# Optimization experiments

Measured on AMD Instinct MI355X. Metric: run time of the kernel, lower is better.

## Reference

```python
import jax, jax.numpy as jnp
import numpy as np

N_NODES = 100000
N_EDGES = 1600000
IN_FEAT = 256
HIDDEN = 64
N_CLASSES = 16


def gcn_conv(x, edge_index, W, b):
    """PyG GCNConv: add self-loops, symmetric normalization, linear+aggregate."""
    n = x.shape[0]
    src, dst = edge_index[0], edge_index[1]
    loops = jnp.arange(n, dtype=src.dtype)
    src = jnp.concatenate([src, loops])
    dst = jnp.concatenate([dst, loops])
    # in-degree on graph with self-loops
    deg = jax.ops.segment_sum(jnp.ones(src.shape[0], dtype=x.dtype), dst, num_segments=n)
    dinv = jnp.where(deg > 0, jax.lax.rsqrt(deg), 0.0)
    h = x @ W                                  # [N, out]
    norm = dinv[src] * dinv[dst]               # [E+N]
    msg = h[src] * norm[:, None]                # gather + scale (memory-bound)
    out = jax.ops.segment_sum(msg, dst, num_segments=n)  # scatter-add
    return out + b


def setup_inputs() -> dict:
    key = jax.random.key(0)
    ks = jax.random.split(key, 5)
    x = jax.random.normal(ks[0], (N_NODES, IN_FEAT), dtype=jnp.float32)
    edge_index = jax.random.randint(ks[1], (2, N_EDGES), 0, N_NODES, dtype=jnp.int64)
    W1 = jax.random.normal(ks[2], (IN_FEAT, HIDDEN), dtype=jnp.float32) * (1.0 / np.sqrt(IN_FEAT))
    b1 = jnp.zeros((HIDDEN,), dtype=jnp.float32)
    W2 = jax.random.normal(ks[3], (HIDDEN, N_CLASSES), dtype=jnp.float32) * (1.0 / np.sqrt(HIDDEN))
    b2 = jnp.zeros((N_CLASSES,), dtype=jnp.float32)
    return {"x": x, "edge_index": edge_index, "W1": W1, "b1": b1, "W2": W2, "b2": b2}


def reference(x, edge_index, W1, b1, W2, b2):
    h = gcn_conv(x, edge_index, W1, b1)
    h = jax.nn.relu(h)
    # dropout p=0.5 is identity in eval mode (training=False)
    out = gcn_conv(h, edge_index, W2, b2)
    return out
```

## Files before the change

kernel.cpp:

```cpp
#include <hip/hip_runtime.h>

#define NN 100000
#define NE 1600000
#define FIN 256
#define FH 64
#define FC 16

#define SCAN_CHUNK 1024
#define NB_SCAN ((NN + SCAN_CHUNK - 1) / SCAN_CHUNK)
#define NB_COUNT ((NE + 255) / 256)
#define NB_GEMM1 ((NN + 127) / 128)
#define NB_FUSED (9 * NB_GEMM1)

typedef int v2i __attribute__((ext_vector_type(2)));
typedef short s16x8 __attribute__((ext_vector_type(8)));
typedef float f32x4 __attribute__((ext_vector_type(4)));

__device__ __forceinline__ float4 fma4(float4 v, float w, float4 a) {
    a.x = fmaf(v.x, w, a.x); a.y = fmaf(v.y, w, a.y);
    a.z = fmaf(v.z, w, a.z); a.w = fmaf(v.w, w, a.w);
    return a;
}
__device__ __forceinline__ float4 add4(float4 a, float4 v) {
    a.x += v.x; a.y += v.y; a.z += v.z; a.w += v.w;
    return a;
}
__device__ __forceinline__ float4 xor_add4(float4 r, int m) {
    r.x += __shfl_xor(r.x, m, 64); r.y += __shfl_xor(r.y, m, 64);
    r.z += __shfl_xor(r.z, m, 64); r.w += __shfl_xor(r.w, m, 64);
    return r;
}

__device__ __forceinline__ unsigned short bf16rne(float f) {
    unsigned u = __float_as_uint(f);
    u += 0x7FFFu + ((u >> 16) & 1u);
    return (unsigned short)(u >> 16);
}

__device__ __forceinline__ void split8(const float* f, s16x8& hi, s16x8& lo) {
    #pragma unroll
    for (int i = 0; i < 8; i++) {
        unsigned u = __float_as_uint(f[i]);
        unsigned short h = (unsigned short)((u + 0x7FFFu + ((u >> 16) & 1u)) >> 16);
        float l = f[i] - __uint_as_float((unsigned)h << 16);
        unsigned ul = __float_as_uint(l);
        hi[i] = (short)h;
        lo[i] = (short)((ul + 0x7FFFu + ((ul >> 16) & 1u)) >> 16);
    }
}

__device__ __forceinline__ int eidx(const int* __restrict__ ei, int f, int pos) {
    return f ? ei[2 * pos] : ei[pos];
}

__global__ __launch_bounds__(256) void prep_k(const int* __restrict__ ei,
                                              int* __restrict__ flag,
                                              const float* __restrict__ W,
                                              unsigned short* __restrict__ Whi,
                                              unsigned short* __restrict__ Wlo) {
    int b = blockIdx.x;
    if (b == 8) {
        if (threadIdx.x == 0) {
            int z = (ei[1] == 0) & (ei[3] == 0) & (ei[5] == 0) & (ei[7] == 0);
            *flag = z;
        }
        return;
    }
    int slot = b * 256 + threadIdx.x;
    int l = slot & 63;
    int c = (slot >> 6) & 3;
    int s = slot >> 8;
    int k0 = s * 32 + (l >> 4) * 8;
    int col = c * 16 + (l & 15);
    #pragma unroll
    for (int i = 0; i < 8; i++) {
        float f = W[(k0 + i) * FH + col];
        unsigned short h = bf16rne(f);
        float lres = f - __uint_as_float((unsigned)h << 16);
        Whi[slot * 8 + i] = h;
        Wlo[slot * 8 + i] = bf16rne(lres);
    }
}

__global__ __launch_bounds__(256, 4) void fused_k(const int* __restrict__ ei,
                                                  const int* __restrict__ flag,
                                                  int* __restrict__ deg,
                                                  v2i* __restrict__ packed,
                                                  const float* __restrict__ x,
                                                  const unsigned short* __restrict__ Whi,
                                                  const unsigned short* __restrict__ Wlo,
                                                  float* __restrict__ h1) {
    const int b = blockIdx.x;
    if ((b % 9) != 8) {
        int cb = (b / 9) * 8 + (b % 9);
        if (cb >= NB_COUNT) return;
        int e = cb * 256 + threadIdx.x;
        if (e >= NE) return;
        int f = *flag;
        int s = eidx(ei, f, e);
        int d = eidx(ei, f, NE + e);
        int r = atomicAdd(&deg[d], 1);
        v2i p; p.x = s; p.y = d | (r << 17);
        packed[e] = p;
        return;
    }
    const int t = threadIdx.x;
    const int lane = t & 63;
    const int wid = t >> 6;
    const int mb = (b / 9) * 128 + wid * 32;
    const int lr = lane & 15;
    const int lk = (lane >> 4) * 8;

    int ra0 = mb + lr;
    int ra1 = mb + 16 + lr;
    const float* pa0 = x + (size_t)(ra0 < NN ? ra0 : NN - 1) * FIN + lk;
    const float* pa1 = x + (size_t)(ra1 < NN ? ra1 : NN - 1) * FIN + lk;

    f32x4 acc[2][4] = {};

    for (int s = 0; s < 8; s++) {
        float fa0[8], fa1[8];
        float4 q;
        q = *(const float4*)(pa0 + s * 32);
        fa0[0] = q.x; fa0[1] = q.y; fa0[2] = q.z; fa0[3] = q.w;
        q = *(const float4*)(pa0 + s * 32 + 4);
        fa0[4] = q.x; fa0[5] = q.y; fa0[6] = q.z; fa0[7] = q.w;
        q = *(const float4*)(pa1 + s * 32);
        fa1[0] = q.x; fa1[1] = q.y; fa1[2] = q.z; fa1[3] = q.w;
        q = *(const float4*)(pa1 + s * 32 + 4);
        fa1[4] = q.x; fa1[5] = q.y; fa1[6] = q.z; fa1[7] = q.w;

        s16x8 a0h, a0l, a1h, a1l;
        split8(fa0, a0h, a0l);
        split8(fa1, a1h, a1l);

        #pragma unroll
        for (int c = 0; c < 4; c++) {
            s16x8 wh = *(const s16x8*)&Whi[((s * 4 + c) * 64 + lane) * 8];
            s16x8 wl = *(const s16x8*)&Wlo[((s * 4 + c) * 64 + lane) * 8];
            acc[0][c] = __builtin_amdgcn_mfma_f32_16x16x32_bf16(a0h, wh, acc[0][c], 0, 0, 0);
            acc[0][c] = __builtin_amdgcn_mfma_f32_16x16x32_bf16(a0l, wh, acc[0][c], 0, 0, 0);
            acc[0][c] = __builtin_amdgcn_mfma_f32_16x16x32_bf16(a0h, wl, acc[0][c], 0, 0, 0);
            acc[1][c] = __builtin_amdgcn_mfma_f32_16x16x32_bf16(a1h, wh, acc[1][c], 0, 0, 0);
            acc[1][c] = __builtin_amdgcn_mfma_f32_16x16x32_bf16(a1l, wh, acc[1][c], 0, 0, 0);
            acc[1][c] = __builtin_amdgcn_mfma_f32_16x16x32_bf16(a1h, wl, acc[1][c], 0, 0, 0);
        }
    }
    #pragma unroll
    for (int r = 0; r < 2; r++) {
        int rowb = mb + 16 * r + (lane >> 4) * 4;
        #pragma unroll
        for (int c = 0; c < 4; c++) {
            #pragma unroll
            for (int v = 0; v < 4; v++) {
                int row = rowb + v;
                if (row < NN)
                    h1[(size_t)row * FH + 16 * c + lr] = acc[r][c][v];
            }
        }
    }
}

__global__ __launch_bounds__(256) void scan_sum_k(const int* __restrict__ deg,
                                                  int* __restrict__ partial,
                                                  float* __restrict__ dinv) {
    __shared__ int red[256];
    int b = blockIdx.x, t = threadIdx.x;
    int base = b * SCAN_CHUNK + t * 4;
    int s = 0;
    #pragma unroll
    for (int i = 0; i < 4; i++) {
        int idx = base + i;
        if (idx < NN) {
            int dv = deg[idx];
            s += dv;
            dinv[idx] = rsqrtf((float)(dv + 1));
        }
    }
    red[t] = s;
    __syncthreads();
    for (int off = 128; off > 0; off >>= 1) {
        if (t < off) red[t] += red[t + off];
        __syncthreads();
    }
    if (t == 0) partial[b] = red[0];
}

__global__ __launch_bounds__(256) void scale1_k(float* __restrict__ h1,
                                                const float* __restrict__ dinv) {
    int i = blockIdx.x * 256 + threadIdx.x;
    if (i >= NN * 16) return;
    int row = i >> 4;
    float d = dinv[row];
    float4 v = *(const float4*)&h1[i * 4];
    v.x *= d; v.y *= d; v.z *= d; v.w *= d;
    *(float4*)&h1[i * 4] = v;
}

__global__ __launch_bounds__(128) void scan_part_k(int* __restrict__ partial) {
    __shared__ int s[128];
    int t = threadIdx.x;
    int v = (t < NB_SCAN) ? partial[t] : 0;
    s[t] = v; __syncthreads();
    for (int off = 1; off < 128; off <<= 1) {
        int u = (t >= off) ? s[t - off] : 0;
        __syncthreads();
        s[t] += u;
        __syncthreads();
    }
    if (t < NB_SCAN) partial[t] = s[t] - v;
}

__global__ __launch_bounds__(256) void scan_out_k(const int* __restrict__ deg,
                                                  const int* __restrict__ partial,
                                                  int* __restrict__ row_start) {
    __shared__ int s[256];
    int b = blockIdx.x, t = threadIdx.x;
    int base = b * SCAN_CHUNK + t * 4;
    int v[4]; int sum = 0;
    #pragma unroll
    for (int i = 0; i < 4; i++) {
        int idx = base + i;
        v[i] = (idx < NN) ? deg[idx] : 0;
        sum += v[i];
    }
    s[t] = sum; __syncthreads();
    for (int off = 1; off < 256; off <<= 1) {
        int u = (t >= off) ? s[t - off] : 0;
        __syncthreads();
        s[t] += u;
        __syncthreads();
    }
    int run = partial[b] + s[t] - sum;
    #pragma unroll
    for (int i = 0; i < 4; i++) {
        int idx = base + i;
        if (idx < NN) {
            row_start[idx] = run;
            run += v[i];
            if (idx == NN - 1) row_start[NN] = run;
        }
    }
}

__global__ __launch_bounds__(256) void fill_k(const v2i* __restrict__ packed,
                                              const int* __restrict__ row_start,
                                              int* __restrict__ csr) {
    int e = blockIdx.x * 256 + threadIdx.x;
    if (e >= NE) return;
    v2i p = __builtin_nontemporal_load(&packed[e]);
    int d = p.y & 0x1FFFF;
    int r = ((unsigned)p.y) >> 17;
    csr[row_start[d] + r] = p.x;
}

__global__ __launch_bounds__(256) void agg1g_k(const int* __restrict__ csr,
                                               const int* __restrict__ row_start,
                                               const float* __restrict__ h1,
                                               const float* __restrict__ dinv,
                                               const float* __restrict__ b1,
                                               const float* __restrict__ W2,
                                               float* __restrict__ h2) {
    __shared__ float sW2[FH * FC];
    __shared__ float sp[4][FH];
    const int t = threadIdx.x;
    #pragma unroll
    for (int i = 0; i < 4; i++) sW2[t + 256 * i] = W2[t + 256 * i];
    __syncthreads();

    int wid = t >> 6;
    int n = blockIdx.x * 4 + wid;
    int lane = t & 63;
    if (n >= NN) return;
    int sg = lane >> 4;
    int fl = lane & 15;
    int s0 = row_start[n], s1 = row_start[n + 1];
    float4 A = make_float4(0.f, 0.f, 0.f, 0.f);
    float4 B = make_float4(0.f, 0.f, 0.f, 0.f);
    float4 C = make_float4(0.f, 0.f, 0.f, 0.f);
    float4 D = make_float4(0.f, 0.f, 0.f, 0.f);
    for (int j0 = s0; j0 < s1; j0 += 64) {
        int idx = j0 + lane;
        int sl = (idx < s1) ? csr[idx] : 0;
        int cnt = s1 - j0; if (cnt > 64) cnt = 64;
        int j = 0;
        for (; j + 16 <= cnt; j += 16) {
            int eA = __shfl(sl, j + sg, 64);
            int eB = __shfl(sl, j + 4 + sg, 64);
            int eC = __shfl(sl, j + 8 + sg, 64);
            int eD = __shfl(sl, j + 12 + sg, 64);
            float4 vA = *(const float4*)&h1[eA * FH + fl * 4];
            float4 vB = *(const float4*)&h1[eB * FH + fl * 4];
            float4 vC = *(const float4*)&h1[eC * FH + fl * 4];
            float4 vD = *(const float4*)&h1[eD * FH + fl * 4];
            A = add4(A, vA); B = add4(B, vB);
            C = add4(C, vC); D = add4(D, vD);
        }
        if (j + 8 <= cnt) {
            int eA = __shfl(sl, j + sg, 64);
            int eB = __shfl(sl, j + 4 + sg, 64);
            float4 vA = *(const float4*)&h1[eA * FH + fl * 4];
            float4 vB = *(const float4*)&h1[eB * FH + fl * 4];
            A = add4(A, vA); B = add4(B, vB);
            j += 8;
        }
        if (j + 4 <= cnt) {
            int eA = __shfl(sl, j + sg, 64);
            float4 vA = *(const float4*)&h1[eA * FH + fl * 4];
            A = add4(A, vA);
            j += 4;
        }
        int rem = cnt - j;
        if (rem > 0) {
            int jj = j + (sg < rem ? sg : 0);
            int eA = __shfl(sl, jj, 64);
            float wA = (sg < rem) ? 1.f : 0.f;
            float4 vA = *(const float4*)&h1[eA * FH + fl * 4];
            A = fma4(vA, wA, A);
        }
    }
    float4 r = add4(add4(A, B), add4(C, D));
    r = xor_add4(r, 16);
    r = xor_add4(r, 32);
    float dn = dinv[n];
    if (sg == 0) {
        float4 self = *(const float4*)&h1[n * FH + fl * 4];
        float4 bq = *(const float4*)&b1[fl * 4];
        float4 p;
        p.x = fmaxf(fmaf(r.x + self.x, dn, bq.x), 0.f);
        p.y = fmaxf(fmaf(r.y + self.y, dn, bq.y), 0.f);
        p.z = fmaxf(fmaf(r.z + self.z, dn, bq.z), 0.f);
        p.w = fmaxf(fmaf(r.w + self.w, dn, bq.w), 0.f);
        *(float4*)&sp[wid][fl * 4] = p;
    }
    __builtin_amdgcn_s_waitcnt(0);
    if (lane < FC) {
        float o = 0.f;
        #pragma unroll 8
        for (int k = 0; k < FH; k++)
            o = fmaf(sp[wid][k], sW2[k * FC + lane], o);
        h2[n * FC + lane] = o * dn;
    }
}

__global__ __launch_bounds__(256) void agg2_k(const int* __restrict__ csr,
                                              const int* __restrict__ row_start,
                                              const float* __restrict__ h2,
                                              const float* __restrict__ dinv,
                                              const float* __restrict__ b2,
                                              float* __restrict__ out) {
    const int t = threadIdx.x;
    int n = blockIdx.x * 16 + (t >> 4);
    int l16 = t & 15;
    int base = t & 48;
    int q = (t >> 2) & 3;
    int c = t & 3;
    if (n >= NN) return;
    int s0 = row_start[n], s1 = row_start[n + 1];
    float4 A = make_float4(0.f, 0.f, 0.f, 0.f);
    float4 B = make_float4(0.f, 0.f, 0.f, 0.f);
    float4 C = make_float4(0.f, 0.f, 0.f, 0.f);
    float4 D = make_float4(0.f, 0.f, 0.f, 0.f);
    for (int j0 = s0; j0 < s1; j0 += 16) {
        int idx = j0 + l16;
        int sl = (idx < s1) ? csr[idx] : 0;
        int cnt = s1 - j0; if (cnt > 16) cnt = 16;
        int j = 0;
        if (j + 16 <= cnt) {
            int eA = __shfl(sl, base + j + q, 64);
            int eB = __shfl(sl, base + j + 4 + q, 64);
            int eC = __shfl(sl, base + j + 8 + q, 64);
            int eD = __shfl(sl, base + j + 12 + q, 64);
            float4 vA = *(const float4*)&h2[eA * FC + c * 4];
            float4 vB = *(const float4*)&h2[eB * FC + c * 4];
            float4 vC = *(const float4*)&h2[eC * FC + c * 4];
            float4 vD = *(const float4*)&h2[eD * FC + c * 4];
            A = add4(A, vA); B = add4(B, vB);
            C = add4(C, vC); D = add4(D, vD);
            j += 16;
        }
        if (j + 8 <= cnt) {
            int eA = __shfl(sl, base + j + q, 64);
            int eB = __shfl(sl, base + j + 4 + q, 64);
            float4 vA = *(const float4*)&h2[eA * FC + c * 4];
            float4 vB = *(const float4*)&h2[eB * FC + c * 4];
            A = add4(A, vA); B = add4(B, vB);
            j += 8;
        }
        if (j + 4 <= cnt) {
            int eA = __shfl(sl, base + j + q, 64);
            float4 vA = *(const float4*)&h2[eA * FC + c * 4];
            A = add4(A, vA);
            j += 4;
        }
        int rem = cnt - j;
        if (rem > 0) {
            int jj = base + j + (q < rem ? q : 0);
            int eA = __shfl(sl, jj, 64);
            float wA = (q < rem) ? 1.f : 0.f;
            float4 vA = *(const float4*)&h2[eA * FC + c * 4];
            A = fma4(vA, wA, A);
        }
    }
    float4 r = add4(add4(A, B), add4(C, D));
    r = xor_add4(r, 4);
    r = xor_add4(r, 8);
    if (q == 0) {
        float dn = dinv[n];
        float4 self = *(const float4*)&h2[n * FC + c * 4];
        float4 bq = *(const float4*)&b2[c * 4];
        float4 p;
        p.x = fmaf(r.x + self.x, dn, bq.x);
        p.y = fmaf(r.y + self.y, dn, bq.y);
        p.z = fmaf(r.z + self.z, dn, bq.z);
        p.w = fmaf(r.w + self.w, dn, bq.w);
        *(float4*)&out[n * FC + c * 4] = p;
    }
}

extern "C" void kernel_launch(void* const* d_in, const int* in_sizes, int n_in,
                              void* d_out, int out_size, void* d_ws, size_t ws_size,
                              hipStream_t stream) {
    const float* x  = (const float*)d_in[0];
    const int*   ei = (const int*)d_in[1];
    const float* W1 = (const float*)d_in[2];
    const float* b1 = (const float*)d_in[3];
    const float* W2 = (const float*)d_in[4];
    const float* b2 = (const float*)d_in[5];
    float* out = (float*)d_out;

    char* ws = (char*)d_ws;
    int*   deg       = (int*)(ws + 0);
    int*   row_start = (int*)(ws + 512 * 1024);
    float* dinv      = (float*)(ws + 1024 * 1024);
    int*   flag      = (int*)(ws + 1536 * 1024);
    int*   partial   = (int*)(ws + 1540 * 1024);
    unsigned short* Whi = (unsigned short*)(ws + 1544 * 1024);
    unsigned short* Wlo = (unsigned short*)(ws + 1584 * 1024);
    int*   csr       = (int*)(ws + 2ull * 1024 * 1024);
    float* h1        = (float*)(ws + 9ull * 1024 * 1024);
    v2i*   packed    = (v2i*)(ws + 35ull * 1024 * 1024);
    float* h2        = (float*)(ws + 35ull * 1024 * 1024);

    prep_k<<<9, 256, 0, stream>>>(ei, flag, W1, Whi, Wlo);
    (void)hipMemsetAsync(deg, 0, NN * sizeof(int), stream);
    fused_k<<<NB_FUSED, 256, 0, stream>>>(ei, flag, deg, packed, x, Whi, Wlo, h1);
    scan_sum_k<<<NB_SCAN, 256, 0, stream>>>(deg, partial, dinv);
    scale1_k<<<(NN * 16 + 255) / 256, 256, 0, stream>>>(h1, dinv);
    scan_part_k<<<1, 128, 0, stream>>>(partial);
    scan_out_k<<<NB_SCAN, 256, 0, stream>>>(deg, partial, row_start);
    fill_k<<<(NE + 255) / 256, 256, 0, stream>>>(packed, row_start, csr);

    agg1g_k<<<(NN + 3) / 4, 256, 0, stream>>>(csr, row_start, h1, dinv, b1, W2, h2);
    agg2_k<<<(NN + 15) / 16, 256, 0, stream>>>(csr, row_start, h2, dinv, b2, out);
}
```

Baseline: 353.9 us.

## Vectorize edge counting and CSR fill, fuse h1 scaling into scan-sum kernel

The degree-counting blocks now have each thread handle four edges with vector loads of the edge indices and packed stores, so the fused kernel's block interleave ratio drops from 8:1 to 2:1. The fill kernel handles two edges per thread with a 16-byte nontemporal load. The separate scale1 kernel is removed, and h1 rows are scaled by dinv inside scan_sum_k using a shared-memory copy of dinv. This saves one launch and one pass over h1. The cost is fewer, heavier blocks and a scan kernel that now streams about 25 MB of h1 with only 98 blocks, which may underuse the GPU.

```diff
diff --git a/kernel.cpp b/kernel.cpp
--- a/kernel.cpp
+++ b/kernel.cpp
@@ -8,11 +8,12 @@
 
 #define SCAN_CHUNK 1024
 #define NB_SCAN ((NN + SCAN_CHUNK - 1) / SCAN_CHUNK)
-#define NB_COUNT ((NE + 255) / 256)
+#define NB_COUNT ((NE / 4 + 255) / 256)
 #define NB_GEMM1 ((NN + 127) / 128)
-#define NB_FUSED (9 * NB_GEMM1)
+#define NB_FUSED (3 * NB_GEMM1)
 
 typedef int v2i __attribute__((ext_vector_type(2)));
+typedef int v4i __attribute__((ext_vector_type(4)));
 typedef short s16x8 __attribute__((ext_vector_type(8)));
 typedef float f32x4 __attribute__((ext_vector_type(4)));
 
@@ -47,10 +48,6 @@
         hi[i] = (short)h;
         lo[i] = (short)((ul + 0x7FFFu + ((ul >> 16) & 1u)) >> 16);
     }
-}
-
-__device__ __forceinline__ int eidx(const int* __restrict__ ei, int f, int pos) {
-    return f ? ei[2 * pos] : ei[pos];
 }
 
 __global__ __launch_bounds__(256) void prep_k(const int* __restrict__ ei,
@@ -91,23 +88,43 @@
                                                   const unsigned short* __restrict__ Wlo,
                                                   float* __restrict__ h1) {
     const int b = blockIdx.x;
-    if ((b % 9) != 8) {
-        int cb = (b / 9) * 8 + (b % 9);
+    if ((b % 3) != 2) {
+        int cb = (b / 3) * 2 + (b % 3);
         if (cb >= NB_COUNT) return;
-        int e = cb * 256 + threadIdx.x;
+        int e = (cb * 256 + threadIdx.x) * 4;
         if (e >= NE) return;
         int f = *flag;
-        int s = eidx(ei, f, e);
-        int d = eidx(ei, f, NE + e);
-        int r = atomicAdd(&deg[d], 1);
-        v2i p; p.x = s; p.y = d | (r << 17);
-        packed[e] = p;
+        int s0, s1, s2, s3, d0, d1, d2, d3;
+        if (f) {
+            v4i a = *(const v4i*)&ei[2 * e];
+            v4i b2 = *(const v4i*)&ei[2 * e + 4];
+            s0 = a.x; s1 = a.z; s2 = b2.x; s3 = b2.z;
+            v4i c = *(const v4i*)&ei[2 * (NE + e)];
+            v4i d = *(const v4i*)&ei[2 * (NE + e) + 4];
+            d0 = c.x; d1 = c.z; d2 = d.x; d3 = d.z;
+        } else {
+            v4i a = *(const v4i*)&ei[e];
+            s0 = a.x; s1 = a.y; s2 = a.z; s3 = a.w;
+            v4i c = *(const v4i*)&ei[NE + e];
+            d0 = c.x; d1 = c.y; d2 = c.z; d3 = c.w;
+        }
+        int r0 = atomicAdd(&deg[d0], 1);
+        int r1 = atomicAdd(&deg[d1], 1);
+        int r2 = atomicAdd(&deg[d2], 1);
+        int r3 = atomicAdd(&deg[d3], 1);
+        v4i pa, pb;
+        pa.x = s0; pa.y = d0 | (r0 << 17);
+        pa.z = s1; pa.w = d1 | (r1 << 17);
+        pb.x = s2; pb.y = d2 | (r2 << 17);
+        pb.z = s3; pb.w = d3 | (r3 << 17);
+        *(v4i*)&packed[e] = pa;
+        *(v4i*)&packed[e + 2] = pb;
         return;
     }
     const int t = threadIdx.x;
     const int lane = t & 63;
     const int wid = t >> 6;
-    const int mb = (b / 9) * 128 + wid * 32;
+    const int mb = (b / 3) * 128 + wid * 32;
     const int lr = lane & 15;
     const int lk = (lane >> 4) * 8;
 
@@ -163,38 +180,44 @@
 
 __global__ __launch_bounds__(256) void scan_sum_k(const int* __restrict__ deg,
                                                   int* __restrict__ partial,
-                                                  float* __restrict__ dinv) {
+                                                  float* __restrict__ dinv,
+                                                  float* __restrict__ h1) {
     __shared__ int red[256];
+    __shared__ float sdv[SCAN_CHUNK];
     int b = blockIdx.x, t = threadIdx.x;
     int base = b * SCAN_CHUNK + t * 4;
     int s = 0;
     #pragma unroll
     for (int i = 0; i < 4; i++) {
         int idx = base + i;
+        float dv = 0.f;
         if (idx < NN) {
-            int dv = deg[idx];
-            s += dv;
-            dinv[idx] = rsqrtf((float)(dv + 1));
-        }
+            int d = deg[idx];
+            s += d;
+            dv = rsqrtf((float)(d + 1));
+            dinv[idx] = dv;
+        }
+        sdv[t * 4 + i] = dv;
     }
     red[t] = s;
     __syncthreads();
+    #pragma unroll 4
+    for (int it = 0; it < 64; it++) {
+        int q = it * 256 + t;
+        int rl = q >> 4;
+        int row = b * SCAN_CHUNK + rl;
+        if (row < NN) {
+            float d = sdv[rl];
+            float4 v = *(const float4*)&h1[(size_t)row * FH + (q & 15) * 4];
+            v.x *= d; v.y *= d; v.z *= d; v.w *= d;
+            *(float4*)&h1[(size_t)row * FH + (q & 15) * 4] = v;
+        }
+    }
     for (int off = 128; off > 0; off >>= 1) {
         if (t < off) red[t] += red[t + off];
         __syncthreads();
     }
     if (t == 0) partial[b] = red[0];
-}
-
-__global__ __launch_bounds__(256) void scale1_k(float* __restrict__ h1,
-                                                const float* __restrict__ dinv) {
-    int i = blockIdx.x * 256 + threadIdx.x;
-    if (i >= NN * 16) return;
-    int row = i >> 4;
-    float d = dinv[row];
-    float4 v = *(const float4*)&h1[i * 4];
-    v.x *= d; v.y *= d; v.z *= d; v.w *= d;
-    *(float4*)&h1[i * 4] = v;
 }
 
 __global__ __launch_bounds__(128) void scan_part_k(int* __restrict__ partial) {
@@ -243,15 +266,18 @@
     }
 }
 
-__global__ __launch_bounds__(256) void fill_k(const v2i* __restrict__ packed,
+__global__ __launch_bounds__(256) void fill_k(const int* __restrict__ packed,
                                               const int* __restrict__ row_start,
                                               int* __restrict__ csr) {
-    int e = blockIdx.x * 256 + threadIdx.x;
+    int e = (blockIdx.x * 256 + threadIdx.x) * 2;
     if (e >= NE) return;
-    v2i p = __builtin_nontemporal_load(&packed[e]);
-    int d = p.y & 0x1FFFF;
-    int r = ((unsigned)p.y) >> 17;
-    csr[row_start[d] + r] = p.x;
+    v4i p = __builtin_nontemporal_load((const v4i*)&packed[2 * e]);
+    int d0 = p.y & 0x1FFFF;
+    int r0 = ((unsigned)p.y) >> 17;
+    int d1 = p.w & 0x1FFFF;
+    int r1 = ((unsigned)p.w) >> 17;
+    csr[row_start[d0] + r0] = p.x;
+    csr[row_start[d1] + r1] = p.z;
 }
 
 __global__ __launch_bounds__(256) void agg1g_k(const int* __restrict__ csr,
@@ -445,11 +471,10 @@
     prep_k<<<9, 256, 0, stream>>>(ei, flag, W1, Whi, Wlo);
     (void)hipMemsetAsync(deg, 0, NN * sizeof(int), stream);
     fused_k<<<NB_FUSED, 256, 0, stream>>>(ei, flag, deg, packed, x, Whi, Wlo, h1);
-    scan_sum_k<<<NB_SCAN, 256, 0, stream>>>(deg, partial, dinv);
-    scale1_k<<<(NN * 16 + 255) / 256, 256, 0, stream>>>(h1, dinv);
+    scan_sum_k<<<NB_SCAN, 256, 0, stream>>>(deg, partial, dinv, h1);
     scan_part_k<<<1, 128, 0, stream>>>(partial);
     scan_out_k<<<NB_SCAN, 256, 0, stream>>>(deg, partial, row_start);
-    fill_k<<<(NE + 255) / 256, 256, 0, stream>>>(packed, row_start, csr);
+    fill_k<<<(NE / 2 + 255) / 256, 256, 0, stream>>>((const int*)packed, row_start, csr);
 
     agg1g_k<<<(NN + 3) / 4, 256, 0, stream>>>(csr, row_start, h1, dinv, b1, W2, h2);
     agg2_k<<<(NN + 15) / 16, 256, 0, stream>>>(csr, row_start, h2, dinv, b2, out);
```

Result: slower. 368.9 us (+4.2%).

## Replace atomic-degree CSR build with two-level bucket sort by destination

Applied to the files above, without the earlier changes.

Builds the CSR with a two-level counting sort instead of global per-node atomics plus a packed fill pass. Edges are first histogrammed and scattered into 512-node buckets using shared-memory atomics. A per-bucket kernel then builds local histograms, row starts, dinv and the CSR in LDS, and also applies the dinv scaling to h1. This removes the global atomic contention, the memset, several scan kernels and the separate scale pass, but unfuses the GEMM from edge counting and reads edge_index twice. CSR order within a row is no longer deterministic.

```diff
diff --git a/kernel.cpp b/kernel.cpp
--- a/kernel.cpp
+++ b/kernel.cpp
@@ -6,13 +6,15 @@
 #define FH 64
 #define FC 16
 
-#define SCAN_CHUNK 1024
-#define NB_SCAN ((NN + SCAN_CHUNK - 1) / SCAN_CHUNK)
-#define NB_COUNT ((NE + 255) / 256)
+#define NPB 512
+#define NBKT ((NN + NPB - 1) / NPB)
+#define NBLK 256
+#define CHUNK (NE / NBLK)
+#define CAP 12288
 #define NB_GEMM1 ((NN + 127) / 128)
-#define NB_FUSED (9 * NB_GEMM1)
 
 typedef int v2i __attribute__((ext_vector_type(2)));
+typedef int v4i __attribute__((ext_vector_type(4)));
 typedef short s16x8 __attribute__((ext_vector_type(8)));
 typedef float f32x4 __attribute__((ext_vector_type(4)));
 
@@ -36,7 +38,6 @@
     u += 0x7FFFu + ((u >> 16) & 1u);
     return (unsigned short)(u >> 16);
 }
-
 __device__ __forceinline__ void split8(const float* f, s16x8& hi, s16x8& lo) {
     #pragma unroll
     for (int i = 0; i < 8; i++) {
@@ -47,10 +48,6 @@
         hi[i] = (short)h;
         lo[i] = (short)((ul + 0x7FFFu + ((ul >> 16) & 1u)) >> 16);
     }
-}
-
-__device__ __forceinline__ int eidx(const int* __restrict__ ei, int f, int pos) {
-    return f ? ei[2 * pos] : ei[pos];
 }
 
 __global__ __launch_bounds__(256) void prep_k(const int* __restrict__ ei,
@@ -82,32 +79,14 @@
     }
 }
 
-__global__ __launch_bounds__(256, 4) void fused_k(const int* __restrict__ ei,
-                                                  const int* __restrict__ flag,
-                                                  int* __restrict__ deg,
-                                                  v2i* __restrict__ packed,
-                                                  const float* __restrict__ x,
+__global__ __launch_bounds__(256, 4) void gemm1_k(const float* __restrict__ x,
                                                   const unsigned short* __restrict__ Whi,
                                                   const unsigned short* __restrict__ Wlo,
                                                   float* __restrict__ h1) {
-    const int b = blockIdx.x;
-    if ((b % 9) != 8) {
-        int cb = (b / 9) * 8 + (b % 9);
-        if (cb >= NB_COUNT) return;
-        int e = cb * 256 + threadIdx.x;
-        if (e >= NE) return;
-        int f = *flag;
-        int s = eidx(ei, f, e);
-        int d = eidx(ei, f, NE + e);
-        int r = atomicAdd(&deg[d], 1);
-        v2i p; p.x = s; p.y = d | (r << 17);
-        packed[e] = p;
-        return;
-    }
     const int t = threadIdx.x;
     const int lane = t & 63;
     const int wid = t >> 6;
-    const int mb = (b / 9) * 128 + wid * 32;
+    const int mb = blockIdx.x * 128 + wid * 32;
     const int lr = lane & 15;
     const int lk = (lane >> 4) * 8;
 
@@ -161,97 +140,142 @@
     }
 }
 
-__global__ __launch_bounds__(256) void scan_sum_k(const int* __restrict__ deg,
-                                                  int* __restrict__ partial,
-                                                  float* __restrict__ dinv) {
-    __shared__ int red[256];
-    int b = blockIdx.x, t = threadIdx.x;
-    int base = b * SCAN_CHUNK + t * 4;
-    int s = 0;
-    #pragma unroll
-    for (int i = 0; i < 4; i++) {
-        int idx = base + i;
-        if (idx < NN) {
-            int dv = deg[idx];
-            s += dv;
-            dinv[idx] = rsqrtf((float)(dv + 1));
-        }
-    }
-    red[t] = s;
-    __syncthreads();
-    for (int off = 128; off > 0; off >>= 1) {
-        if (t < off) red[t] += red[t + off];
-        __syncthreads();
-    }
-    if (t == 0) partial[b] = red[0];
-}
-
-__global__ __launch_bounds__(256) void scale1_k(float* __restrict__ h1,
-                                                const float* __restrict__ dinv) {
-    int i = blockIdx.x * 256 + threadIdx.x;
-    if (i >= NN * 16) return;
-    int row = i >> 4;
-    float d = dinv[row];
-    float4 v = *(const float4*)&h1[i * 4];
-    v.x *= d; v.y *= d; v.z *= d; v.w *= d;
-    *(float4*)&h1[i * 4] = v;
-}
-
-__global__ __launch_bounds__(128) void scan_part_k(int* __restrict__ partial) {
-    __shared__ int s[128];
-    int t = threadIdx.x;
-    int v = (t < NB_SCAN) ? partial[t] : 0;
-    s[t] = v; __syncthreads();
-    for (int off = 1; off < 128; off <<= 1) {
+__global__ __launch_bounds__(256) void hist_k(const int* __restrict__ ei,
+                                              const int* __restrict__ flag,
+                                              int* __restrict__ cnt) {
+    __shared__ int hist[NBKT];
+    const int t = threadIdx.x, blk = blockIdx.x;
+    for (int j = t; j < NBKT; j += 256) hist[j] = 0;
+    __syncthreads();
+    int f = *flag;
+    int base = blk * CHUNK;
+    if (f) {
+        for (int i = t; i < CHUNK; i += 256) {
+            v2i p = *(const v2i*)&ei[2 * (NE + base + i)];
+            atomicAdd(&hist[p.x >> 9], 1);
+        }
+    } else {
+        for (int i = t; i < CHUNK; i += 256) {
+            int d = ei[NE + base + i];
+            atomicAdd(&hist[d >> 9], 1);
+        }
+    }
+    __syncthreads();
+    for (int j = t; j < NBKT; j += 256) cnt[j * NBLK + blk] = hist[j];
+}
+
+__global__ __launch_bounds__(1024) void scanoff_k(int* __restrict__ cnt,
+                                                  int* __restrict__ bucketBase) {
+    __shared__ int s[1024];
+    const int t = threadIdx.x;
+    const int SEG = (NBKT * NBLK) / 1024;
+    int base = t * SEG;
+    int sum = 0;
+    for (int i = 0; i < SEG; i++) sum += cnt[base + i];
+    s[t] = sum; __syncthreads();
+    for (int off = 1; off < 1024; off <<= 1) {
         int u = (t >= off) ? s[t - off] : 0;
         __syncthreads();
         s[t] += u;
         __syncthreads();
     }
-    if (t < NB_SCAN) partial[t] = s[t] - v;
-}
-
-__global__ __launch_bounds__(256) void scan_out_k(const int* __restrict__ deg,
-                                                  const int* __restrict__ partial,
-                                                  int* __restrict__ row_start) {
-    __shared__ int s[256];
-    int b = blockIdx.x, t = threadIdx.x;
-    int base = b * SCAN_CHUNK + t * 4;
-    int v[4]; int sum = 0;
-    #pragma unroll
-    for (int i = 0; i < 4; i++) {
-        int idx = base + i;
-        v[i] = (idx < NN) ? deg[idx] : 0;
-        sum += v[i];
-    }
-    s[t] = sum; __syncthreads();
+    int run = s[t] - sum;
+    for (int i = 0; i < SEG; i++) {
+        int g = base + i;
+        int v = cnt[g];
+        cnt[g] = run;
+        if ((g & (NBLK - 1)) == 0) bucketBase[g / NBLK] = run;
+        run += v;
+    }
+    if (t == 0) bucketBase[NBKT] = NE;
+}
+
+__global__ __launch_bounds__(256) void scat_k(const int* __restrict__ ei,
+                                              const int* __restrict__ flag,
+                                              const int* __restrict__ cnt,
+                                              int* __restrict__ sorted) {
+    __shared__ int offl[NBKT];
+    const int t = threadIdx.x, blk = blockIdx.x;
+    for (int j = t; j < NBKT; j += 256) offl[j] = cnt[j * NBLK + blk];
+    __syncthreads();
+    int f = *flag;
+    int base = blk * CHUNK;
+    if (f) {
+        for (int i = t; i < CHUNK; i += 256) {
+            int e = base + i;
+            v2i ps = *(const v2i*)&ei[2 * e];
+            v2i pd = *(const v2i*)&ei[2 * (NE + e)];
+            int s = ps.x, d = pd.x;
+            int pos = atomicAdd(&offl[d >> 9], 1);
+            sorted[pos] = s | ((d & (NPB - 1)) << 17);
+        }
+    } else {
+        for (int i = t; i < CHUNK; i += 256) {
+            int e = base + i;
+            int s = ei[e], d = ei[NE + e];
+            int pos = atomicAdd(&offl[d >> 9], 1);
+            sorted[pos] = s | ((d & (NPB - 1)) << 17);
+        }
+    }
+}
+
+__global__ __launch_bounds__(256) void bucket_k(const int* __restrict__ sorted,
+                                                const int* __restrict__ bucketBase,
+                                                int* __restrict__ csr,
+                                                int* __restrict__ row_start,
+                                                float* __restrict__ dinv,
+                                                float* __restrict__ h1) {
+    __shared__ int stash[CAP];
+    __shared__ int hist[NPB];
+    __shared__ int startl[NPB];
+    __shared__ int cursor[NPB];
+    __shared__ int ss[256];
+    const int t = threadIdx.x, b = blockIdx.x;
+    const int nb0 = b * NPB;
+    const int ncnt = (NN - nb0 < NPB) ? (NN - nb0) : NPB;
+    const int ebase = bucketBase[b];
+    const int ecnt = bucketBase[b + 1] - ebase;
+
+    hist[t] = 0; hist[t + 256] = 0;
+    __syncthreads();
+    for (int i = t; i < ecnt; i += 256) {
+        int v = sorted[ebase + i];
+        if (i < CAP) stash[i] = v;
+        atomicAdd(&hist[v >> 17], 1);
+    }
+    __syncthreads();
+    int a = hist[2 * t], c = hist[2 * t + 1];
+    int p = a + c;
+    ss[t] = p; __syncthreads();
     for (int off = 1; off < 256; off <<= 1) {
-        int u = (t >= off) ? s[t - off] : 0;
+        int u = (t >= off) ? ss[t - off] : 0;
         __syncthreads();
-        s[t] += u;
+        ss[t] += u;
         __syncthreads();
     }
-    int run = partial[b] + s[t] - sum;
-    #pragma unroll
-    for (int i = 0; i < 4; i++) {
-        int idx = base + i;
-        if (idx < NN) {
-            row_start[idx] = run;
-            run += v[i];
-            if (idx == NN - 1) row_start[NN] = run;
-        }
-    }
-}
-
-__global__ __launch_bounds__(256) void fill_k(const v2i* __restrict__ packed,
-                                              const int* __restrict__ row_start,
-                                              int* __restrict__ csr) {
-    int e = blockIdx.x * 256 + threadIdx.x;
-    if (e >= NE) return;
-    v2i p = __builtin_nontemporal_load(&packed[e]);
-    int d = p.y & 0x1FFFF;
-    int r = ((unsigned)p.y) >> 17;
-    csr[row_start[d] + r] = p.x;
+    int ex = ss[t] - p;
+    startl[2 * t] = ex;       startl[2 * t + 1] = ex + a;
+    cursor[2 * t] = ex;       cursor[2 * t + 1] = ex + a;
+    __syncthreads();
+    for (int j = t; j < ncnt; j += 256) {
+        row_start[nb0 + j] = ebase + startl[j];
+        dinv[nb0 + j] = rsqrtf((float)(hist[j] + 1));
+    }
+    if (b == 0 && t == 0) row_start[NN] = NE;
+    for (int i = t; i < ecnt; i += 256) {
+        int v = (i < CAP) ? stash[i] : sorted[ebase + i];
+        int dl = v >> 17;
+        int r = atomicAdd(&cursor[dl], 1);
+        csr[ebase + r] = v & 0x1FFFF;
+    }
+    for (int q = t; q < ncnt * 16; q += 256) {
+        int rl = q >> 4;
+        float dv = rsqrtf((float)(hist[rl] + 1));
+        size_t off = (size_t)(nb0 + rl) * FH + (q & 15) * 4;
+        float4 v = *(const float4*)&h1[off];
+        v.x *= dv; v.y *= dv; v.z *= dv; v.w *= dv;
+        *(float4*)&h1[off] = v;
+    }
 }
 
 __global__ __launch_bounds__(256) void agg1g_k(const int* __restrict__ csr,
@@ -430,26 +454,24 @@
     float* out = (float*)d_out;
 
     char* ws = (char*)d_ws;
-    int*   deg       = (int*)(ws + 0);
-    int*   row_start = (int*)(ws + 512 * 1024);
-    float* dinv      = (float*)(ws + 1024 * 1024);
-    int*   flag      = (int*)(ws + 1536 * 1024);
-    int*   partial   = (int*)(ws + 1540 * 1024);
-    unsigned short* Whi = (unsigned short*)(ws + 1544 * 1024);
-    unsigned short* Wlo = (unsigned short*)(ws + 1584 * 1024);
-    int*   csr       = (int*)(ws + 2ull * 1024 * 1024);
-    float* h1        = (float*)(ws + 9ull * 1024 * 1024);
-    v2i*   packed    = (v2i*)(ws + 35ull * 1024 * 1024);
-    float* h2        = (float*)(ws + 35ull * 1024 * 1024);
+    int*   row_start  = (int*)(ws + 0);
+    float* dinv       = (float*)(ws + 512ull * 1024);
+    int*   flag       = (int*)(ws + 1024ull * 1024);
+    int*   bucketBase = (int*)(ws + 1028ull * 1024);
+    unsigned short* Whi = (unsigned short*)(ws + 1040ull * 1024);
+    unsigned short* Wlo = (unsigned short*)(ws + 1072ull * 1024);
+    int*   cnt        = (int*)(ws + 1104ull * 1024);
+    int*   csr        = (int*)(ws + 2048ull * 1024);
+    int*   sorted     = (int*)(ws + 9216ull * 1024);
+    float* h2         = (float*)(ws + 9216ull * 1024);
+    float* h1         = (float*)(ws + 16384ull * 1024);
 
     prep_k<<<9, 256, 0, stream>>>(ei, flag, W1, Whi, Wlo);
-    (void)hipMemsetAsync(deg, 0, NN * sizeof(int), stream);
-    fused_k<<<NB_FUSED, 256, 0, stream>>>(ei, flag, deg, packed, x, Whi, Wlo, h1);
-    scan_sum_k<<<NB_SCAN, 256, 0, stream>>>(deg, partial, dinv);
-    scale1_k<<<(NN * 16 + 255) / 256, 256, 0, stream>>>(h1, dinv);
-    scan_part_k<<<1, 128, 0, stream>>>(partial);
-    scan_out_k<<<NB_SCAN, 256, 0, stream>>>(deg, partial, row_start);
-    fill_k<<<(NE + 255) / 256, 256, 0, stream>>>(packed, row_start, csr);
+    gemm1_k<<<NB_GEMM1, 256, 0, stream>>>(x, Whi, Wlo, h1);
+    hist_k<<<NBLK, 256, 0, stream>>>(ei, flag, cnt);
+    scanoff_k<<<1, 1024, 0, stream>>>(cnt, bucketBase);
+    scat_k<<<NBLK, 256, 0, stream>>>(ei, flag, cnt, sorted);
+    bucket_k<<<NBKT, 256, 0, stream>>>(sorted, bucketBase, csr, row_start, dinv, h1);
 
     agg1g_k<<<(NN + 3) / 4, 256, 0, stream>>>(csr, row_start, h1, dinv, b1, W2, h2);
     agg2_k<<<(NN + 15) / 16, 256, 0, stream>>>(csr, row_start, h2, dinv, b2, out);
```

Result: slower. 398.2 us (+12.5%).
